# Kernel optimization log

Measured on AMD Instinct MI355X. Metric: run time of the kernel, lower is better.

## Reference

```python
import jax, jax.numpy as jnp
import numpy as np

N = 1024
H = 256
EH = max(16, H // 2)  # edge_hidden


def _lin(key, fan_in, fan_out):
    kw, kb = jax.random.split(key)
    s = 1.0 / np.sqrt(fan_in)
    W = jax.random.uniform(kw, (fan_in, fan_out), jnp.float32, -s, s)
    b = jax.random.uniform(kb, (fan_out,), jnp.float32, -s, s)
    return W, b


def setup_inputs() -> dict:
    key = jax.random.key(0)
    ks = jax.random.split(key, 14)
    inp = {
        'h': jax.random.normal(ks[0], (N, H), jnp.float32),
        'delta_local': jax.random.normal(ks[1], (N, 3), jnp.float32),
        't_emb': jax.random.normal(ks[2], (N, 3), jnp.float32),
        'x_current': jax.random.normal(ks[3], (N, 3), jnp.float32),
        'frames': jax.random.normal(ks[4], (N, 3, 3), jnp.float32),
    }
    inp['np1_w'], inp['np1_b'] = _lin(ks[5], H + 6, H)
    inp['np2_w'], inp['np2_b'] = _lin(ks[6], H, H)
    inp['src_w'], inp['src_b'] = _lin(ks[7], H, 1)
    inp['dst_w'], inp['dst_b'] = _lin(ks[8], H, 1)
    inp['ns_w'], inp['ns_b'] = _lin(ks[9], H, 1)
    inp['eg1_w'], inp['eg1_b'] = _lin(ks[10], 4, EH)
    inp['eg2_w'], inp['eg2_b'] = _lin(ks[11], EH, 1)
    inp['out1_w'], inp['out1_b'] = _lin(ks[12], H + 6, H)
    inp['out2_w'], inp['out2_b'] = _lin(ks[13], H, 3)
    return inp


def reference(h, delta_local, t_emb, x_current, frames,
              np1_w, np1_b, np2_w, np2_b,
              src_w, src_b, dst_w, dst_b, ns_w, ns_b,
              eg1_w, eg1_b, eg2_w, eg2_b,
              out1_w, out1_b, out2_w, out2_b):
    silu = jax.nn.silu
    # node_proj: two Linear+SiLU on [h, delta_local, t_emb]
    node_feat = jnp.concatenate([h, delta_local, t_emb], axis=-1)  # [N, H+6]
    node_hidden = silu(silu(node_feat @ np1_w + np1_b) @ np2_w + np2_b)  # [N, H]

    # relative positions in each node's local frame
    rel = x_current[None, :, :] - x_current[:, None, :]             # [N, N, 3], rel[n,m]=x[m]-x[n]
    rel_local = jnp.einsum('nji,nmj->nmi', frames, rel)             # frames^T @ rel
    dist = jnp.linalg.norm(rel_local, axis=-1, keepdims=True)       # [N, N, 1]
    edge_feat = jnp.concatenate([rel_local, dist], axis=-1)         # [N, N, 4]

    # edge-gated attention logits: src + dst + per-edge MLP score
    src = (node_hidden @ src_w + src_b)                             # [N, 1]
    dst = (node_hidden @ dst_w + dst_b)                             # [N, 1]
    edge_logit = silu(edge_feat @ eg1_w + eg1_b) @ eg2_w + eg2_b    # [N, N, 1]
    logits = src[:, None, 0] + dst[None, :, 0] + edge_logit[..., 0] # [N, N]

    eye = jnp.eye(N, dtype=bool)
    logits = jnp.where(eye, -10000.0, logits)
    attn = jax.nn.softmax(logits, axis=1)
    attn = jnp.where(eye, 0.0, attn)
    attn = attn / jnp.maximum(attn.sum(axis=1, keepdims=True), 1e-6)

    ns = jax.nn.sigmoid(node_hidden @ ns_w + ns_b)[:, 0]            # [N]
    local_messages = jnp.einsum('nm,m,nmi->ni', attn, ns, rel_local)  # [N, 3]

    update_feat = jnp.concatenate([node_hidden, delta_local, local_messages], axis=-1)
    local_update = silu(update_feat @ out1_w + out1_b) @ out2_w + out2_b  # [N, 3]
    return local_update + 0.25 * local_messages
```

## Files before the change

kernel.cpp:

```cpp
#include <hip/hip_runtime.h>

#define N 1024
#define H 256
#define EH 128

__device__ __forceinline__ float fast_silu(float x) {
    float u = __builtin_amdgcn_exp2f(x * -1.44269504088896340736f);
    return x * __builtin_amdgcn_rcpf(1.0f + u);
}

__global__ __launch_bounds__(1024) void k_node(
    const float* __restrict__ h, const float* __restrict__ dl, const float* __restrict__ temb,
    const float* __restrict__ np1_w, const float* __restrict__ np1_b,
    const float* __restrict__ np2_w, const float* __restrict__ np2_b,
    const float* __restrict__ src_w, const float* __restrict__ src_b,
    const float* __restrict__ dst_w, const float* __restrict__ dst_b,
    const float* __restrict__ ns_w, const float* __restrict__ ns_b,
    const float* __restrict__ eg1_w, const float* __restrict__ eg1_b,
    const float* __restrict__ eg2_w,
    float* __restrict__ nh, float* __restrict__ srcv, float* __restrict__ dstv,
    float* __restrict__ nsv, float* __restrict__ wp)
{
    __shared__ float feat[4][264];
    __shared__ float sred[4][4][256];
    __shared__ float gred[4][3][4];
    const int tid = threadIdx.x;
    const int j   = tid & 255;
    const int seg = tid >> 8;
    const int n0  = blockIdx.x * 4;

    if (blockIdx.x == 0 && tid < EH) {
        const float NL2E = -1.44269504088896340736f;
        const float NLN2 = -0.69314718055994530942f;
        float4 a;
        a.x = NL2E * eg1_w[0 * EH + tid];
        a.y = NL2E * eg1_w[1 * EH + tid];
        a.z = NL2E * eg1_w[2 * EH + tid];
        a.w = NL2E * eg1_w[3 * EH + tid];
        ((float4*)wp)[tid * 2 + 0] = a;
        float4 b;
        b.x = NL2E * eg1_b[tid];
        b.y = 1.0f / (NLN2 * eg2_w[tid]);
        b.z = 0.0f; b.w = 0.0f;
        ((float4*)wp)[tid * 2 + 1] = b;
    }

    for (int idx = tid; idx < 4 * 264; idx += 1024) {
        int t = idx / 264, i = idx % 264;
        int n = n0 + t;
        float v = 0.0f;
        if (i < H)            v = h[n * H + i];
        else if (i < H + 3)   v = dl[n * 3 + (i - H)];
        else if (i < H + 6)   v = temb[n * 3 + (i - H - 3)];
        feat[t][i] = v;
    }
    __syncthreads();

    {
        float a0 = 0.f, a1 = 0.f, a2 = 0.f, a3 = 0.f;
        const int lo = seg * 66;
        const int hi = lo + ((seg == 3) ? 64 : 66);
        for (int i = lo; i < hi; i += 2) {
            float w0 = np1_w[i * H + j];
            float w1 = np1_w[(i + 1) * H + j];
            float2 f0 = *(const float2*)&feat[0][i];
            float2 f1 = *(const float2*)&feat[1][i];
            float2 f2 = *(const float2*)&feat[2][i];
            float2 f3 = *(const float2*)&feat[3][i];
            a0 = fmaf(f0.x, w0, fmaf(f0.y, w1, a0));
            a1 = fmaf(f1.x, w0, fmaf(f1.y, w1, a1));
            a2 = fmaf(f2.x, w0, fmaf(f2.y, w1, a2));
            a3 = fmaf(f3.x, w0, fmaf(f3.y, w1, a3));
        }
        sred[0][seg][j] = a0;
        sred[1][seg][j] = a1;
        sred[2][seg][j] = a2;
        sred[3][seg][j] = a3;
    }
    __syncthreads();
    {
        float s = sred[seg][0][j] + sred[seg][1][j] + sred[seg][2][j] + sred[seg][3][j] + np1_b[j];
        feat[seg][j] = fast_silu(s);
    }
    __syncthreads();

    {
        float a0 = 0.f, a1 = 0.f, a2 = 0.f, a3 = 0.f;
        const int lo = seg * 64;
        for (int i = lo; i < lo + 64; i += 2) {
            float w0 = np2_w[i * H + j];
            float w1 = np2_w[(i + 1) * H + j];
            float2 f0 = *(const float2*)&feat[0][i];
            float2 f1 = *(const float2*)&feat[1][i];
            float2 f2 = *(const float2*)&feat[2][i];
            float2 f3 = *(const float2*)&feat[3][i];
            a0 = fmaf(f0.x, w0, fmaf(f0.y, w1, a0));
            a1 = fmaf(f1.x, w0, fmaf(f1.y, w1, a1));
            a2 = fmaf(f2.x, w0, fmaf(f2.y, w1, a2));
            a3 = fmaf(f3.x, w0, fmaf(f3.y, w1, a3));
        }
        sred[0][seg][j] = a0;
        sred[1][seg][j] = a1;
        sred[2][seg][j] = a2;
        sred[3][seg][j] = a3;
    }
    __syncthreads();

    float h2 = fast_silu(sred[seg][0][j] + sred[seg][1][j] + sred[seg][2][j] + sred[seg][3][j] + np2_b[j]);
    nh[(n0 + seg) * H + j] = h2;

    {
        float ps = h2 * src_w[j], pd = h2 * dst_w[j], pn = h2 * ns_w[j];
        const int lane = tid & 63, wvl = (tid >> 6) & 3;
#pragma unroll
        for (int o = 32; o > 0; o >>= 1) {
            ps += __shfl_down(ps, o);
            pd += __shfl_down(pd, o);
            pn += __shfl_down(pn, o);
        }
        if (lane == 0) { gred[seg][0][wvl] = ps; gred[seg][1][wvl] = pd; gred[seg][2][wvl] = pn; }
    }
    __syncthreads();
    if (tid < 4) {
        int t = tid;
        float s  = gred[t][0][0] + gred[t][0][1] + gred[t][0][2] + gred[t][0][3] + src_b[0];
        float d  = gred[t][1][0] + gred[t][1][1] + gred[t][1][2] + gred[t][1][3] + dst_b[0];
        float nl = gred[t][2][0] + gred[t][2][1] + gred[t][2][2] + gred[t][2][3] + ns_b[0];
        srcv[n0 + t] = s;
        dstv[n0 + t] = d;
        nsv[n0 + t]  = __builtin_amdgcn_rcpf(1.0f + __builtin_amdgcn_exp2f(nl * -1.44269504088896340736f));
    }
}

__global__ __launch_bounds__(512) void k_edge(
    const float* __restrict__ x, const float* __restrict__ frames,
    const float* __restrict__ srcv, const float* __restrict__ dstv,
    const float* __restrict__ nsv,
    const float* __restrict__ wp,
    const float* __restrict__ eg2_b, float* __restrict__ msg)
{
    __shared__ float rmax[8];
    __shared__ float rsum[8];
    __shared__ float rmsg[3][8];
    const int tid = threadIdx.x;
    const int n = blockIdx.x;

    float F[9];
#pragma unroll
    for (int q = 0; q < 9; q++) F[q] = frames[n * 9 + q];
    const float xn0 = x[n * 3 + 0], xn1 = x[n * 3 + 1], xn2 = x[n * 3 + 2];
    const float src_n = srcv[n];
    const float eg2b = eg2_b[0];

    const int m0 = tid;
    const int m1 = tid + 512;
    float rl00, rl01, rl02, d0, rl10, rl11, rl12, d1, dstm0, dstm1, nsm0, nsm1;
    {
        float rx = x[m0 * 3 + 0] - xn0;
        float ry = x[m0 * 3 + 1] - xn1;
        float rz = x[m0 * 3 + 2] - xn2;
        rl00 = F[0] * rx + F[3] * ry + F[6] * rz;
        rl01 = F[1] * rx + F[4] * ry + F[7] * rz;
        rl02 = F[2] * rx + F[5] * ry + F[8] * rz;
        d0 = sqrtf(rl00 * rl00 + rl01 * rl01 + rl02 * rl02);
        dstm0 = dstv[m0];
        nsm0  = nsv[m0];
    }
    {
        float rx = x[m1 * 3 + 0] - xn0;
        float ry = x[m1 * 3 + 1] - xn1;
        float rz = x[m1 * 3 + 2] - xn2;
        rl10 = F[0] * rx + F[3] * ry + F[6] * rz;
        rl11 = F[1] * rx + F[4] * ry + F[7] * rz;
        rl12 = F[2] * rx + F[5] * ry + F[8] * rz;
        d1 = sqrtf(rl10 * rl10 + rl11 * rl11 + rl12 * rl12);
        dstm1 = dstv[m1];
        nsm1  = nsv[m1];
    }

    float acc0 = 0.f, acc1 = 0.f;
    const float4* __restrict__ Wq = (const float4*)wp;

#define KSTEP(Xa, Xb)                                                                    \
    {                                                                                    \
        float t20 = fmaf(rl00, Xa.x, fmaf(rl01, Xa.y, fmaf(rl02, Xa.z, fmaf(d0, Xa.w, Xb.x)))); \
        float t21 = fmaf(rl10, Xa.x, fmaf(rl11, Xa.y, fmaf(rl12, Xa.z, fmaf(d1, Xa.w, Xb.x)))); \
        float u0 = __builtin_amdgcn_exp2f(t20);                                          \
        float u1 = __builtin_amdgcn_exp2f(t21);                                          \
        float v0 = fmaf(u0, Xb.y, Xb.y);                                                 \
        float v1 = fmaf(u1, Xb.y, Xb.y);                                                 \
        float r0 = __builtin_amdgcn_rcpf(v0);                                            \
        float r1 = __builtin_amdgcn_rcpf(v1);                                            \
        acc0 = fmaf(t20, r0, acc0);                                                      \
        acc1 = fmaf(t21, r1, acc1);                                                      \
    }

    float4 A0 = Wq[0], A1 = Wq[1], A2 = Wq[2], A3 = Wq[3],
           A4 = Wq[4], A5 = Wq[5], A6 = Wq[6], A7 = Wq[7];
    float4 B0, B1, B2, B3, B4, B5, B6, B7;

    for (int c = 0; c < 32; c += 2) {
        {
            const int i1 = (c + 1) * 8;
            B0 = Wq[i1 + 0]; B1 = Wq[i1 + 1]; B2 = Wq[i1 + 2]; B3 = Wq[i1 + 3];
            B4 = Wq[i1 + 4]; B5 = Wq[i1 + 5]; B6 = Wq[i1 + 6]; B7 = Wq[i1 + 7];
        }
        KSTEP(A0, A1) KSTEP(A2, A3) KSTEP(A4, A5) KSTEP(A6, A7)
        {
            const int i2 = ((c + 2 < 32) ? (c + 2) : 31) * 8;
            A0 = Wq[i2 + 0]; A1 = Wq[i2 + 1]; A2 = Wq[i2 + 2]; A3 = Wq[i2 + 3];
            A4 = Wq[i2 + 4]; A5 = Wq[i2 + 5]; A6 = Wq[i2 + 6]; A7 = Wq[i2 + 7];
        }
        KSTEP(B0, B1) KSTEP(B2, B3) KSTEP(B4, B5) KSTEP(B6, B7)
    }
#undef KSTEP

    const float base_n = src_n + eg2b;
    float lg0 = (m0 == n) ? -10000.0f : (base_n + dstm0 + acc0);
    float lg1 = (m1 == n) ? -10000.0f : (base_n + dstm1 + acc1);

    const int lane = tid & 63, wv = tid >> 6;
    float mx = fmaxf(lg0, lg1);
#pragma unroll
    for (int o = 32; o > 0; o >>= 1) mx = fmaxf(mx, __shfl_down(mx, o));
    if (lane == 0) rmax[wv] = mx;
    __syncthreads();
    mx = rmax[0];
#pragma unroll
    for (int q = 1; q < 8; q++) mx = fmaxf(mx, rmax[q]);

    float p0 = __builtin_amdgcn_exp2f((lg0 - mx) * 1.44269504088896340736f);
    float p1 = __builtin_amdgcn_exp2f((lg1 - mx) * 1.44269504088896340736f);
    float s = p0 + p1;
#pragma unroll
    for (int o = 32; o > 0; o >>= 1) s += __shfl_down(s, o);
    if (lane == 0) rsum[wv] = s;
    __syncthreads();
    float S = rsum[0] + rsum[1] + rsum[2] + rsum[3] + rsum[4] + rsum[5] + rsum[6] + rsum[7];
    float inv = 1.0f / S;

    float w0 = p0 * inv * nsm0;
    float w1 = p1 * inv * nsm1;
    float a0 = fmaf(w0, rl00, w1 * rl10);
    float a1 = fmaf(w0, rl01, w1 * rl11);
    float a2 = fmaf(w0, rl02, w1 * rl12);
#pragma unroll
    for (int o = 32; o > 0; o >>= 1) {
        a0 += __shfl_down(a0, o);
        a1 += __shfl_down(a1, o);
        a2 += __shfl_down(a2, o);
    }
    if (lane == 0) { rmsg[0][wv] = a0; rmsg[1][wv] = a1; rmsg[2][wv] = a2; }
    __syncthreads();
    if (tid < 3) {
        float v = 0.f;
#pragma unroll
        for (int q = 0; q < 8; q++) v += rmsg[tid][q];
        msg[n * 3 + tid] = v;
    }
}

__global__ __launch_bounds__(1024) void k_out(
    const float* __restrict__ nh, const float* __restrict__ dl, const float* __restrict__ msg,
    const float* __restrict__ out1_w, const float* __restrict__ out1_b,
    const float* __restrict__ out2_w, const float* __restrict__ out2_b,
    float* __restrict__ out)
{
    __shared__ float feat[4][264];
    __shared__ float sred[4][4][256];
    __shared__ float gred[4][3][4];
    const int tid = threadIdx.x;
    const int j   = tid & 255;
    const int seg = tid >> 8;
    const int n0  = blockIdx.x * 4;

    for (int idx = tid; idx < 4 * 264; idx += 1024) {
        int t = idx / 264, i = idx % 264;
        int n = n0 + t;
        float v = 0.0f;
        if (i < H)          v = nh[n * H + i];
        else if (i < H + 3) v = dl[n * 3 + (i - H)];
        else if (i < H + 6) v = msg[n * 3 + (i - H - 3)];
        feat[t][i] = v;
    }
    __syncthreads();

    {
        float a0 = 0.f, a1 = 0.f, a2 = 0.f, a3 = 0.f;
        const int lo = seg * 66;
        const int hi = lo + ((seg == 3) ? 64 : 66);
        for (int i = lo; i < hi; i += 2) {
            float w0 = out1_w[i * H + j];
            float w1 = out1_w[(i + 1) * H + j];
            float2 f0 = *(const float2*)&feat[0][i];
            float2 f1 = *(const float2*)&feat[1][i];
            float2 f2 = *(const float2*)&feat[2][i];
            float2 f3 = *(const float2*)&feat[3][i];
            a0 = fmaf(f0.x, w0, fmaf(f0.y, w1, a0));
            a1 = fmaf(f1.x, w0, fmaf(f1.y, w1, a1));
            a2 = fmaf(f2.x, w0, fmaf(f2.y, w1, a2));
            a3 = fmaf(f3.x, w0, fmaf(f3.y, w1, a3));
        }
        sred[0][seg][j] = a0;
        sred[1][seg][j] = a1;
        sred[2][seg][j] = a2;
        sred[3][seg][j] = a3;
    }
    __syncthreads();

    float hv = fast_silu(sred[seg][0][j] + sred[seg][1][j] + sred[seg][2][j] + sred[seg][3][j] + out1_b[j]);
    {
        float w0 = out2_w[j * 3 + 0], w1 = out2_w[j * 3 + 1], w2 = out2_w[j * 3 + 2];
        float p0 = hv * w0, p1 = hv * w1, p2 = hv * w2;
        const int lane = tid & 63, wvl = (tid >> 6) & 3;
#pragma unroll
        for (int o = 32; o > 0; o >>= 1) {
            p0 += __shfl_down(p0, o);
            p1 += __shfl_down(p1, o);
            p2 += __shfl_down(p2, o);
        }
        if (lane == 0) { gred[seg][0][wvl] = p0; gred[seg][1][wvl] = p1; gred[seg][2][wvl] = p2; }
    }
    __syncthreads();
    if (tid < 12) {
        int t = tid / 3, d = tid % 3;
        float v = gred[t][d][0] + gred[t][d][1] + gred[t][d][2] + gred[t][d][3] + out2_b[d];
        int n = n0 + t;
        out[n * 3 + d] = v + 0.25f * msg[n * 3 + d];
    }
}

extern "C" void kernel_launch(void* const* d_in, const int* in_sizes, int n_in,
                              void* d_out, int out_size, void* d_ws, size_t ws_size,
                              hipStream_t stream) {
    const float* h      = (const float*)d_in[0];
    const float* dl     = (const float*)d_in[1];
    const float* temb   = (const float*)d_in[2];
    const float* x      = (const float*)d_in[3];
    const float* fr     = (const float*)d_in[4];
    const float* np1_w  = (const float*)d_in[5];
    const float* np1_b  = (const float*)d_in[6];
    const float* np2_w  = (const float*)d_in[7];
    const float* np2_b  = (const float*)d_in[8];
    const float* src_w  = (const float*)d_in[9];
    const float* src_b  = (const float*)d_in[10];
    const float* dst_w  = (const float*)d_in[11];
    const float* dst_b  = (const float*)d_in[12];
    const float* ns_w   = (const float*)d_in[13];
    const float* ns_b   = (const float*)d_in[14];
    const float* eg1_w  = (const float*)d_in[15];
    const float* eg1_b  = (const float*)d_in[16];
    const float* eg2_w  = (const float*)d_in[17];
    const float* eg2_b  = (const float*)d_in[18];
    const float* out1_w = (const float*)d_in[19];
    const float* out1_b = (const float*)d_in[20];
    const float* out2_w = (const float*)d_in[21];
    const float* out2_b = (const float*)d_in[22];

    float* ws   = (float*)d_ws;
    float* nh   = ws;
    float* srcv = nh + 1024 * 256;
    float* dstv = srcv + 1024;
    float* nsv  = dstv + 1024;
    float* msg  = nsv + 1024;
    float* wp   = msg + 1024 * 3;

    k_node<<<256, 1024, 0, stream>>>(h, dl, temb, np1_w, np1_b, np2_w, np2_b,
                                     src_w, src_b, dst_w, dst_b, ns_w, ns_b,
                                     eg1_w, eg1_b, eg2_w,
                                     nh, srcv, dstv, nsv, wp);
    k_edge<<<1024, 512, 0, stream>>>(x, fr, srcv, dstv, nsv, wp, eg2_b, msg);
    k_out<<<256, 1024, 0, stream>>>(nh, dl, msg, out1_w, out1_b, out2_w, out2_b, (float*)d_out);
}
```

Measured before the change: 163.3 us.

## Compute edge MLP first layer with bf16 MFMA instead of scalar FMAs

```diff
diff --git a/kernel.cpp b/kernel.cpp
--- a/kernel.cpp
+++ b/kernel.cpp
@@ -4,9 +4,17 @@
 #define H 256
 #define EH 128
 
+typedef __attribute__((ext_vector_type(8))) short bf16x8;
+typedef __attribute__((ext_vector_type(4))) float f32x4;
+
 __device__ __forceinline__ float fast_silu(float x) {
     float u = __builtin_amdgcn_exp2f(x * -1.44269504088896340736f);
     return x * __builtin_amdgcn_rcpf(1.0f + u);
+}
+
+__device__ __forceinline__ unsigned short f2bf(float f) {
+    unsigned u = __builtin_bit_cast(unsigned, f);
+    return (unsigned short)((u + 0x7FFFu + ((u >> 16) & 1u)) >> 16);
 }
 
 __global__ __launch_bounds__(1024) void k_node(
@@ -40,7 +48,7 @@
         ((float4*)wp)[tid * 2 + 0] = a;
         float4 b;
         b.x = NL2E * eg1_b[tid];
-        b.y = 1.0f / (NLN2 * eg2_w[tid]);
+        b.y = NLN2 * eg2_w[tid];
         b.z = 0.0f; b.w = 0.0f;
         ((float4*)wp)[tid * 2 + 1] = b;
     }
@@ -139,10 +147,16 @@
     const float* __restrict__ wp,
     const float* __restrict__ eg2_b, float* __restrict__ msg)
 {
+    __shared__ ushort4 efeat[1024];
+    __shared__ float eacc[1024];
     __shared__ float rmax[8];
     __shared__ float rsum[8];
     __shared__ float rmsg[3][8];
-    const int tid = threadIdx.x;
+    const int tid  = threadIdx.x;
+    const int lane = tid & 63;
+    const int wv   = tid >> 6;
+    const int wbase = wv * 128;
+    const int col  = lane & 15;
     const int n = blockIdx.x;
 
     float F[9];
@@ -152,8 +166,8 @@
     const float src_n = srcv[n];
     const float eg2b = eg2_b[0];
 
-    const int m0 = tid;
-    const int m1 = tid + 512;
+    const int m0 = wbase + lane;
+    const int m1 = wbase + 64 + lane;
     float rl00, rl01, rl02, d0, rl10, rl11, rl12, d1, dstm0, dstm1, nsm0, nsm1;
     {
         float rx = x[m0 * 3 + 0] - xn0;
@@ -177,49 +191,81 @@
         dstm1 = dstv[m1];
         nsm1  = nsv[m1];
     }
-
-    float acc0 = 0.f, acc1 = 0.f;
-    const float4* __restrict__ Wq = (const float4*)wp;
-
-#define KSTEP(Xa, Xb)                                                                    \
-    {                                                                                    \
-        float t20 = fmaf(rl00, Xa.x, fmaf(rl01, Xa.y, fmaf(rl02, Xa.z, fmaf(d0, Xa.w, Xb.x)))); \
-        float t21 = fmaf(rl10, Xa.x, fmaf(rl11, Xa.y, fmaf(rl12, Xa.z, fmaf(d1, Xa.w, Xb.x)))); \
-        float u0 = __builtin_amdgcn_exp2f(t20);                                          \
-        float u1 = __builtin_amdgcn_exp2f(t21);                                          \
-        float v0 = fmaf(u0, Xb.y, Xb.y);                                                 \
-        float v1 = fmaf(u1, Xb.y, Xb.y);                                                 \
-        float r0 = __builtin_amdgcn_rcpf(v0);                                            \
-        float r1 = __builtin_amdgcn_rcpf(v1);                                            \
-        acc0 = fmaf(t20, r0, acc0);                                                      \
-        acc1 = fmaf(t21, r1, acc1);                                                      \
-    }
-
-    float4 A0 = Wq[0], A1 = Wq[1], A2 = Wq[2], A3 = Wq[3],
-           A4 = Wq[4], A5 = Wq[5], A6 = Wq[6], A7 = Wq[7];
-    float4 B0, B1, B2, B3, B4, B5, B6, B7;
-
-    for (int c = 0; c < 32; c += 2) {
-        {
-            const int i1 = (c + 1) * 8;
-            B0 = Wq[i1 + 0]; B1 = Wq[i1 + 1]; B2 = Wq[i1 + 2]; B3 = Wq[i1 + 3];
-            B4 = Wq[i1 + 4]; B5 = Wq[i1 + 5]; B6 = Wq[i1 + 6]; B7 = Wq[i1 + 7];
-        }
-        KSTEP(A0, A1) KSTEP(A2, A3) KSTEP(A4, A5) KSTEP(A6, A7)
-        {
-            const int i2 = ((c + 2 < 32) ? (c + 2) : 31) * 8;
-            A0 = Wq[i2 + 0]; A1 = Wq[i2 + 1]; A2 = Wq[i2 + 2]; A3 = Wq[i2 + 3];
-            A4 = Wq[i2 + 4]; A5 = Wq[i2 + 5]; A6 = Wq[i2 + 6]; A7 = Wq[i2 + 7];
-        }
-        KSTEP(B0, B1) KSTEP(B2, B3) KSTEP(B4, B5) KSTEP(B6, B7)
-    }
-#undef KSTEP
+    {
+        ushort4 u0; u0.x = f2bf(rl00); u0.y = f2bf(rl01); u0.z = f2bf(rl02); u0.w = f2bf(d0);
+        ushort4 u1; u1.x = f2bf(rl10); u1.y = f2bf(rl11); u1.z = f2bf(rl12); u1.w = f2bf(d1);
+        efeat[m0] = u0;
+        efeat[m1] = u1;
+    }
+
+    bf16x8 Bf[8];
+    float bc[8], w2c[8];
+#pragma unroll
+    for (int c = 0; c < 8; c++) {
+        int kout = c * 16 + col;
+        float4 wa = ((const float4*)wp)[kout * 2 + 0];
+        float4 wb = ((const float4*)wp)[kout * 2 + 1];
+        bf16x8 bfv = {0, 0, 0, 0, 0, 0, 0, 0};
+        if (lane < 16) {
+            bfv[0] = (short)f2bf(wa.x);
+            bfv[1] = (short)f2bf(wa.y);
+            bfv[2] = (short)f2bf(wa.z);
+            bfv[3] = (short)f2bf(wa.w);
+        }
+        Bf[c] = bfv;
+        bc[c]  = wb.x;
+        w2c[c] = wb.y;
+    }
+    __syncthreads();
+
+    const f32x4 zc = {0.f, 0.f, 0.f, 0.f};
+#pragma unroll
+    for (int r = 0; r < 8; r++) {
+        ushort4 fvv = efeat[wbase + r * 16 + col];
+        bf16x8 Af = {0, 0, 0, 0, 0, 0, 0, 0};
+        if (lane < 16) {
+            Af[0] = (short)fvv.x; Af[1] = (short)fvv.y;
+            Af[2] = (short)fvv.z; Af[3] = (short)fvv.w;
+        }
+        float p0 = 0.f, p1 = 0.f, p2 = 0.f, p3 = 0.f;
+#pragma unroll
+        for (int c = 0; c < 8; c++) {
+            f32x4 t = __builtin_amdgcn_mfma_f32_16x16x32_bf16(Af, Bf[c], zc, 0, 0, 0);
+            float t20 = t[0] + bc[c];
+            float t21 = t[1] + bc[c];
+            float t22 = t[2] + bc[c];
+            float t23 = t[3] + bc[c];
+            float u0 = __builtin_amdgcn_exp2f(t20);
+            float u1 = __builtin_amdgcn_exp2f(t21);
+            float u2 = __builtin_amdgcn_exp2f(t22);
+            float u3 = __builtin_amdgcn_exp2f(t23);
+            float r0 = __builtin_amdgcn_rcpf(1.0f + u0);
+            float r1 = __builtin_amdgcn_rcpf(1.0f + u1);
+            float r2 = __builtin_amdgcn_rcpf(1.0f + u2);
+            float r3 = __builtin_amdgcn_rcpf(1.0f + u3);
+            p0 = fmaf(t20 * r0, w2c[c], p0);
+            p1 = fmaf(t21 * r1, w2c[c], p1);
+            p2 = fmaf(t22 * r2, w2c[c], p2);
+            p3 = fmaf(t23 * r3, w2c[c], p3);
+        }
+#pragma unroll
+        for (int o = 1; o < 16; o <<= 1) {
+            p0 += __shfl_xor(p0, o);
+            p1 += __shfl_xor(p1, o);
+            p2 += __shfl_xor(p2, o);
+            p3 += __shfl_xor(p3, o);
+        }
+        if ((lane & 15) == 0) {
+            float4 pv; pv.x = p0; pv.y = p1; pv.z = p2; pv.w = p3;
+            *(float4*)&eacc[wbase + r * 16 + (lane >> 4) * 4] = pv;
+        }
+    }
+    __syncthreads();
 
     const float base_n = src_n + eg2b;
-    float lg0 = (m0 == n) ? -10000.0f : (base_n + dstm0 + acc0);
-    float lg1 = (m1 == n) ? -10000.0f : (base_n + dstm1 + acc1);
-
-    const int lane = tid & 63, wv = tid >> 6;
+    float lg0 = (m0 == n) ? -10000.0f : (base_n + dstm0 + eacc[m0]);
+    float lg1 = (m1 == n) ? -10000.0f : (base_n + dstm1 + eacc[m1]);
+
     float mx = fmaxf(lg0, lg1);
 #pragma unroll
     for (int o = 32; o > 0; o >>= 1) mx = fmaxf(mx, __shfl_down(mx, o));
```

New measurement: 166.0 us. Within noise of the previous version (+1.7%).

## Replace hardware exp2 with polynomial exp2 in edge MLP loop

Applied to the files above, without the earlier changes.

```diff
diff --git a/kernel.cpp b/kernel.cpp
--- a/kernel.cpp
+++ b/kernel.cpp
@@ -40,7 +40,7 @@
         ((float4*)wp)[tid * 2 + 0] = a;
         float4 b;
         b.x = NL2E * eg1_b[tid];
-        b.y = 1.0f / (NLN2 * eg2_w[tid]);
+        b.y = NLN2 * eg2_w[tid];
         b.z = 0.0f; b.w = 0.0f;
         ((float4*)wp)[tid * 2 + 1] = b;
     }
@@ -132,7 +132,7 @@
     }
 }
 
-__global__ __launch_bounds__(512) void k_edge(
+__global__ __launch_bounds__(512, 4) void k_edge(
     const float* __restrict__ x, const float* __restrict__ frames,
     const float* __restrict__ srcv, const float* __restrict__ dstv,
     const float* __restrict__ nsv,
@@ -181,37 +181,34 @@
     float acc0 = 0.f, acc1 = 0.f;
     const float4* __restrict__ Wq = (const float4*)wp;
 
+    const float C1 = 0.69314718056f;
+    const float C2 = 0.24022650696f;
+    const float C3 = 0.05550410866f;
+    const float C4 = 0.00961812911f;
+
 #define KSTEP(Xa, Xb)                                                                    \
     {                                                                                    \
         float t20 = fmaf(rl00, Xa.x, fmaf(rl01, Xa.y, fmaf(rl02, Xa.z, fmaf(d0, Xa.w, Xb.x)))); \
         float t21 = fmaf(rl10, Xa.x, fmaf(rl11, Xa.y, fmaf(rl12, Xa.z, fmaf(d1, Xa.w, Xb.x)))); \
-        float u0 = __builtin_amdgcn_exp2f(t20);                                          \
-        float u1 = __builtin_amdgcn_exp2f(t21);                                          \
-        float v0 = fmaf(u0, Xb.y, Xb.y);                                                 \
-        float v1 = fmaf(u1, Xb.y, Xb.y);                                                 \
-        float r0 = __builtin_amdgcn_rcpf(v0);                                            \
-        float r1 = __builtin_amdgcn_rcpf(v1);                                            \
-        acc0 = fmaf(t20, r0, acc0);                                                      \
-        acc1 = fmaf(t21, r1, acc1);                                                      \
-    }
-
-    float4 A0 = Wq[0], A1 = Wq[1], A2 = Wq[2], A3 = Wq[3],
-           A4 = Wq[4], A5 = Wq[5], A6 = Wq[6], A7 = Wq[7];
-    float4 B0, B1, B2, B3, B4, B5, B6, B7;
-
-    for (int c = 0; c < 32; c += 2) {
-        {
-            const int i1 = (c + 1) * 8;
-            B0 = Wq[i1 + 0]; B1 = Wq[i1 + 1]; B2 = Wq[i1 + 2]; B3 = Wq[i1 + 3];
-            B4 = Wq[i1 + 4]; B5 = Wq[i1 + 5]; B6 = Wq[i1 + 6]; B7 = Wq[i1 + 7];
-        }
-        KSTEP(A0, A1) KSTEP(A2, A3) KSTEP(A4, A5) KSTEP(A6, A7)
-        {
-            const int i2 = ((c + 2 < 32) ? (c + 2) : 31) * 8;
-            A0 = Wq[i2 + 0]; A1 = Wq[i2 + 1]; A2 = Wq[i2 + 2]; A3 = Wq[i2 + 3];
-            A4 = Wq[i2 + 4]; A5 = Wq[i2 + 5]; A6 = Wq[i2 + 6]; A7 = Wq[i2 + 7];
-        }
-        KSTEP(B0, B1) KSTEP(B2, B3) KSTEP(B4, B5) KSTEP(B6, B7)
+        float fl0 = __builtin_rintf(t20);                                                \
+        float fl1 = __builtin_rintf(t21);                                                \
+        float fr0 = t20 - fl0;                                                           \
+        float fr1 = t21 - fl1;                                                           \
+        float p0 = fmaf(fr0, fmaf(fr0, fmaf(fr0, fmaf(fr0, C4, C3), C2), C1), 1.0f);     \
+        float p1 = fmaf(fr1, fmaf(fr1, fmaf(fr1, fmaf(fr1, C4, C3), C2), C1), 1.0f);     \
+        float u0 = __builtin_amdgcn_ldexpf(p0, (int)fl0);                                \
+        float u1 = __builtin_amdgcn_ldexpf(p1, (int)fl1);                                \
+        float r0 = __builtin_amdgcn_rcpf(1.0f + u0);                                     \
+        float r1 = __builtin_amdgcn_rcpf(1.0f + u1);                                     \
+        acc0 = fmaf(t20 * Xb.y, r0, acc0);                                               \
+        acc1 = fmaf(t21 * Xb.y, r1, acc1);                                               \
+    }
+
+#pragma unroll 4
+    for (int k = 0; k < EH; k++) {
+        float4 Wa = Wq[k * 2 + 0];
+        float4 Wb = Wq[k * 2 + 1];
+        KSTEP(Wa, Wb)
     }
 #undef KSTEP
 
```

After: 176.1 us. 1.08x slower.
